# Optimization experiments

Measured on AMD Instinct MI355X. Metric: run time of the kernel, lower is better.

Reference implementation:

```python
import jax, jax.numpy as jnp
import numpy as np

N_NODES = 100000
N_EDGES = 1600000
DIM_IN = 128
DIM_OUT = 128


def setup_inputs() -> dict:
    key = jax.random.key(0)
    k_x, k_e, k_w = jax.random.split(key, 3)
    x = jax.random.normal(k_x, (N_NODES, DIM_IN), dtype=jnp.float32)
    edge_index = jax.random.randint(k_e, (2, N_EDGES), 0, N_NODES, dtype=jnp.int64)
    # Glorot-uniform weight like PyG's GCNConv linear layer, stored [d_in, d_out]
    limit = np.sqrt(6.0 / (DIM_IN + DIM_OUT)).astype(np.float32)
    W = jax.random.uniform(k_w, (DIM_IN, DIM_OUT), dtype=jnp.float32, minval=-limit, maxval=limit)
    return {"x": x, "edge_index": edge_index, "W": W}


def reference(x, edge_index, W):
    # PyG GCNConv (bias=False): out = D^{-1/2} (A + I) D^{-1/2} (x @ W)
    N = x.shape[0]
    x_proj = x @ W  # [N, d_out]
    loop = jnp.arange(N, dtype=edge_index.dtype)
    src = jnp.concatenate([edge_index[0], loop])  # message sources (row)
    dst = jnp.concatenate([edge_index[1], loop])  # aggregation targets (col)
    # degree counted at target nodes (edge weight = 1), incl. self loops
    deg = jax.ops.segment_sum(jnp.ones(src.shape, dtype=x.dtype), dst, num_segments=N)
    dis = jnp.where(deg > 0, jax.lax.rsqrt(deg), 0.0)
    norm = dis[src] * dis[dst]  # [E+N]
    msgs = x_proj[src] * norm[:, None]  # [E+N, d_out] gather + scale
    return jax.ops.segment_sum(msgs, dst, num_segments=N)  # scatter-add
```

## Files before the change

kernel.cpp:

```cpp
#include <hip/hip_runtime.h>
#include <hip/hip_bf16.h>

#define DIM 128
#define PCH 4096

typedef __attribute__((ext_vector_type(8))) short bf16x8;
typedef __attribute__((ext_vector_type(4))) float f32x4;

__device__ __forceinline__ float bfu_lo(unsigned u) { return __uint_as_float(u << 16); }
__device__ __forceinline__ float bfu_hi(unsigned u) { return __uint_as_float(u & 0xffff0000u); }
__device__ __forceinline__ unsigned short f2bf(float f) {
    unsigned u = __float_as_uint(f);
    u += 0x7fffu + ((u >> 16) & 1u);
    return (unsigned short)(u >> 16);
}

__device__ __forceinline__ int edge_at(const void* ei, int idx64, long long pos) {
    return idx64 ? (int)__builtin_nontemporal_load((const long long*)ei + pos)
                 : __builtin_nontemporal_load((const int*)ei + pos);
}

__global__ void init_detect(const unsigned* ei_w, int* flags, unsigned* bcnt, int E) {
    __shared__ unsigned s_or[256];
    int t = threadIdx.x;
    bcnt[t] = 0u;
    bcnt[256 + t] = 0u;
    unsigned o = 0;
    int lim = (E < 4096) ? E : 4096;
    for (int k = t; k < lim; k += 256) o |= ei_w[2 * k + 1];
    s_or[t] = o;
    __syncthreads();
    for (int s = 128; s > 0; s >>= 1) {
        if (t < s) s_or[t] |= s_or[t + s];
        __syncthreads();
    }
    if (t == 0) flags[0] = (s_or[0] == 0u) ? 1 : 0;
}

__global__ __launch_bounds__(256) void hist_pass(const void* ei, const int* flags,
                                                 unsigned* bcnt, int E, int shift) {
    __shared__ unsigned s_h[512];
    int t = threadIdx.x;
    for (int i = t; i < 512; i += 256) s_h[i] = 0u;
    __syncthreads();
    int idx64 = flags[0];
    long long stride = (long long)gridDim.x * 256;
    for (long long e = (long long)blockIdx.x * 256 + t; e < E; e += stride) {
        int d = edge_at(ei, idx64, (long long)E + e);
        atomicAdd(&s_h[d >> shift], 1u);
    }
    __syncthreads();
    for (int i = t; i < 512; i += 256)
        if (s_h[i]) atomicAdd(&bcnt[i], s_h[i]);
}

__global__ void scan_buckets(const unsigned* bcnt, unsigned* bbase, unsigned* bcur) {
    __shared__ unsigned wsum[8];
    int t = threadIdx.x;
    unsigned v = bcnt[t];
    unsigned s = v;
    int lane = t & 63;
#pragma unroll
    for (int off = 1; off < 64; off <<= 1) {
        unsigned u = __shfl_up(s, off, 64);
        if (lane >= off) s += u;
    }
    int w = t >> 6;
    if (lane == 63) wsum[w] = s;
    __syncthreads();
    unsigned woff = 0;
    for (int j = 0; j < w; j++) woff += wsum[j];
    unsigned excl = woff + s - v;
    bbase[t] = excl;
    bcur[t] = excl;
    if (t == 511) bbase[512] = excl + v;
}

__global__ __launch_bounds__(256) void partition(const void* ei, const int* flags,
                                                 unsigned* bcur, long long* pout,
                                                 int E, int B, int shift) {
    __shared__ unsigned s_hist[512], s_off[512], s_gbase[512], s_pref[512];
    __shared__ unsigned wsum[4];
    __shared__ long long s_p[PCH];
    int t = threadIdx.x;
    long long base = (long long)blockIdx.x * PCH;
    for (int i = t; i < 512; i += 256) { s_hist[i] = 0u; s_off[i] = 0u; }
    __syncthreads();
    int idx64 = flags[0];
    int d_[PCH / 256], s_[PCH / 256];
#pragma unroll 4
    for (int j = 0; j < PCH / 256; j++) {
        long long e = base + j * 256 + t;
        if (e < E) {
            d_[j] = edge_at(ei, idx64, (long long)E + e);
            s_[j] = edge_at(ei, idx64, e);
            atomicAdd(&s_hist[d_[j] >> shift], 1u);
        } else d_[j] = -1;
    }
    __syncthreads();
    unsigned v0 = s_hist[2 * t], v1 = s_hist[2 * t + 1];
    unsigned ps = v0 + v1;
    unsigned s = ps;
    int lane = t & 63;
#pragma unroll
    for (int off = 1; off < 64; off <<= 1) {
        unsigned u = __shfl_up(s, off, 64);
        if (lane >= off) s += u;
    }
    int w = t >> 6;
    if (lane == 63) wsum[w] = s;
    __syncthreads();
    unsigned woff = 0;
    for (int j = 0; j < w; j++) woff += wsum[j];
    unsigned excl = woff + s - ps;
    s_pref[2 * t] = excl;
    s_pref[2 * t + 1] = excl + v0;
    __syncthreads();
    for (int i = t; i < B; i += 256)
        if (s_hist[i]) s_gbase[i] = atomicAdd(&bcur[i], s_hist[i]);
#pragma unroll 4
    for (int j = 0; j < PCH / 256; j++)
        if (d_[j] >= 0) {
            int b = d_[j] >> shift;
            unsigned p = s_pref[b] + atomicAdd(&s_off[b], 1u);
            s_p[p] = ((long long)s_[j] << 32) | (unsigned)d_[j];
        }
    __syncthreads();
    long long rem = (long long)E - base;
    unsigned tot = (rem < PCH) ? (unsigned)rem : (unsigned)PCH;
    for (unsigned i = t; i < tot; i += 256) {
        int lo = 0, hi = B - 1;
        while (lo < hi) {
            int mid = (lo + hi + 1) >> 1;
            if (s_pref[mid] <= i) lo = mid; else hi = mid - 1;
        }
        pout[s_gbase[lo] + (i - s_pref[lo])] = s_p[i];
    }
}

__global__ __launch_bounds__(256) void build_csr(const long long* __restrict__ pairs,
                                                 const unsigned* __restrict__ bbase,
                                                 unsigned* deg, unsigned* row_start,
                                                 float* dis, int* col_src,
                                                 int N, int shift) {
    __shared__ unsigned cnt[512], cur[512], pref[512];
    __shared__ unsigned wsum[4];
    int b = blockIdx.x, t = threadIdx.x;
    int npb = 1 << shift;
    if (npb > 512) npb = 512;
    int nodeLo = b << shift;
    unsigned lo = bbase[b], hi = bbase[b + 1];
    for (int i = t; i < npb; i += 256) cnt[i] = 0u;
    __syncthreads();
    for (unsigned e = lo + t; e < hi; e += 256) {
        int d = (int)pairs[e];
        atomicAdd(&cnt[d - nodeLo], 1u);
    }
    __syncthreads();
    unsigned v0 = (2 * t < npb) ? cnt[2 * t] : 0u;
    unsigned v1 = (2 * t + 1 < npb) ? cnt[2 * t + 1] : 0u;
    unsigned ps = v0 + v1;
    unsigned s = ps;
    int lane = t & 63;
#pragma unroll
    for (int off = 1; off < 64; off <<= 1) {
        unsigned u = __shfl_up(s, off, 64);
        if (lane >= off) s += u;
    }
    int w = t >> 6;
    if (lane == 63) wsum[w] = s;
    __syncthreads();
    unsigned woff = 0;
    for (int j = 0; j < w; j++) woff += wsum[j];
    unsigned excl = woff + s - ps;
    if (2 * t < npb) pref[2 * t] = excl;
    if (2 * t + 1 < npb) pref[2 * t + 1] = excl + v0;
    __syncthreads();
    for (int i = t; i < npb; i += 256) {
        int node = nodeLo + i;
        unsigned rs = lo + pref[i];
        if (node < N) {
            unsigned c = cnt[i];
            deg[node] = c;
            row_start[node] = rs;
            dis[node] = rsqrtf((float)c + 1.0f);
        }
        cur[i] = rs;
    }
    __syncthreads();
    for (unsigned e = lo + t; e < hi; e += 256) {
        long long v = pairs[e];
        int d = (int)v;
        int sv = (int)(v >> 32);
        unsigned pos = atomicAdd(&cur[d - nodeLo], 1u);
        col_src[pos] = sv;
    }
}

__global__ void transposeW(const float* W, unsigned short* Wt) {
    int idx = blockIdx.x * 256 + threadIdx.x;
    if (idx < DIM * DIM) {
        int n = idx >> 7, k = idx & 127;
        Wt[idx] = f2bf(W[k * DIM + n]);
    }
}

__global__ __launch_bounds__(256) void gemm_xw(const float* __restrict__ x,
                                               const unsigned short* __restrict__ wt,
                                               const float* __restrict__ dis,
                                               unsigned short* __restrict__ xps, int N) {
    int tid = threadIdx.x;
    int wv = tid >> 6, lane = tid & 63;
    int l15 = lane & 15, quad = lane >> 4;
    int rowBase = blockIdx.x * 128 + wv * 32;

    f32x4 acc[2][8];
#pragma unroll
    for (int mt = 0; mt < 2; mt++)
#pragma unroll
        for (int nt = 0; nt < 8; nt++)
            acc[mt][nt] = (f32x4){0.f, 0.f, 0.f, 0.f};

#pragma unroll
    for (int k0 = 0; k0 < DIM; k0 += 32) {
        bf16x8 aa[2], bb[8];
#pragma unroll
        for (int mt = 0; mt < 2; mt++) {
            int r = rowBase + mt * 16 + l15;
            if (r > N - 1) r = N - 1;
            const float* xf = x + (size_t)r * DIM + k0 + quad * 8;
            float4 u0 = ((const float4*)xf)[0];
            float4 u1 = ((const float4*)xf)[1];
            bf16x8 a;
            a[0] = (short)f2bf(u0.x); a[1] = (short)f2bf(u0.y);
            a[2] = (short)f2bf(u0.z); a[3] = (short)f2bf(u0.w);
            a[4] = (short)f2bf(u1.x); a[5] = (short)f2bf(u1.y);
            a[6] = (short)f2bf(u1.z); a[7] = (short)f2bf(u1.w);
            aa[mt] = a;
        }
#pragma unroll
        for (int nt = 0; nt < 8; nt++)
            bb[nt] = *(const bf16x8*)(wt + (size_t)(nt * 16 + l15) * DIM + k0 + quad * 8);
#pragma unroll
        for (int mt = 0; mt < 2; mt++)
#pragma unroll
            for (int nt = 0; nt < 8; nt++)
                acc[mt][nt] = __builtin_amdgcn_mfma_f32_16x16x32_bf16(bb[nt], aa[mt], acc[mt][nt], 0, 0, 0);
    }

#pragma unroll
    for (int mt = 0; mt < 2; mt++) {
        int r = rowBase + mt * 16 + l15;
        if (r < N) {
            float sc = dis[r];
#pragma unroll
            for (int nt = 0; nt < 8; nt++) {
                int c0 = nt * 16 + quad * 4;
                ushort4 o;
                o.x = f2bf(acc[mt][nt][0] * sc);
                o.y = f2bf(acc[mt][nt][1] * sc);
                o.z = f2bf(acc[mt][nt][2] * sc);
                o.w = f2bf(acc[mt][nt][3] * sc);
                *(ushort4*)(xps + (size_t)r * DIM + c0) = o;
            }
        }
    }
}

__global__ __launch_bounds__(256) void aggregate(const unsigned short* __restrict__ xps,
                                                 const unsigned* __restrict__ row_start,
                                                 const unsigned* __restrict__ deg,
                                                 const float* __restrict__ dis,
                                                 const int* __restrict__ col_src,
                                                 float* __restrict__ out, int N) {
    int wid = (int)((blockIdx.x * 256 + threadIdx.x) >> 6);
    if (wid >= N) return;
    int lane = threadIdx.x & 63;
    int grp = lane >> 4, lin = lane & 15;
    const uint4* xp4 = (const uint4*)xps;

    float acc[8];
#pragma unroll
    for (int j = 0; j < 8; j++) acc[j] = 0.f;

    unsigned rs = row_start[wid];
    unsigned cnt = deg[wid];
    unsigned tot = cnt + 1;

    for (unsigned base = 0; base < tot; base += 64) {
        unsigned slot = base + (unsigned)lane;
        int idx = (slot < cnt) ? col_src[rs + slot] : wid;
        unsigned rem = tot - base; if (rem > 64) rem = 64;
        for (unsigned q = 0; q * 8 < rem; q++) {
            unsigned sl0 = q * 8 + (unsigned)grp;
            unsigned sl1 = sl0 + 4;
            int s0 = __shfl(idx, (int)sl0, 64);
            int s1 = __shfl(idx, (int)sl1, 64);
            float m0 = (sl0 < rem) ? 1.f : 0.f;
            float m1 = (sl1 < rem) ? 1.f : 0.f;
            uint4 v0 = xp4[(size_t)s0 * 16 + lin];
            uint4 v1 = xp4[(size_t)s1 * 16 + lin];
            acc[0] = fmaf(bfu_lo(v0.x), m0, acc[0]);
            acc[1] = fmaf(bfu_hi(v0.x), m0, acc[1]);
            acc[2] = fmaf(bfu_lo(v0.y), m0, acc[2]);
            acc[3] = fmaf(bfu_hi(v0.y), m0, acc[3]);
            acc[4] = fmaf(bfu_lo(v0.z), m0, acc[4]);
            acc[5] = fmaf(bfu_hi(v0.z), m0, acc[5]);
            acc[6] = fmaf(bfu_lo(v0.w), m0, acc[6]);
            acc[7] = fmaf(bfu_hi(v0.w), m0, acc[7]);
            acc[0] = fmaf(bfu_lo(v1.x), m1, acc[0]);
            acc[1] = fmaf(bfu_hi(v1.x), m1, acc[1]);
            acc[2] = fmaf(bfu_lo(v1.y), m1, acc[2]);
            acc[3] = fmaf(bfu_hi(v1.y), m1, acc[3]);
            acc[4] = fmaf(bfu_lo(v1.z), m1, acc[4]);
            acc[5] = fmaf(bfu_hi(v1.z), m1, acc[5]);
            acc[6] = fmaf(bfu_lo(v1.w), m1, acc[6]);
            acc[7] = fmaf(bfu_hi(v1.w), m1, acc[7]);
        }
    }

#pragma unroll
    for (int j = 0; j < 8; j++) {
        acc[j] += __shfl_xor(acc[j], 16, 64);
        acc[j] += __shfl_xor(acc[j], 32, 64);
    }

    float di = dis[wid];
    if (grp < 2) {
        int jb = (grp & 1) * 4;
        float4 o;
        o.x = acc[jb + 0] * di;
        o.y = acc[jb + 1] * di;
        o.z = acc[jb + 2] * di;
        o.w = acc[jb + 3] * di;
        *(float4*)(out + (size_t)wid * DIM + lin * 8 + jb) = o;
    }
}

extern "C" void kernel_launch(void* const* d_in, const int* in_sizes, int n_in,
                              void* d_out, int out_size, void* d_ws, size_t ws_size,
                              hipStream_t stream) {
    const int N = in_sizes[0] / DIM;
    const int E = in_sizes[1] / 2;
    const float* x = (const float*)d_in[0];
    const void* ei = d_in[1];
    const float* W = (const float*)d_in[2];
    float* out = (float*)d_out;

    int shift = 8;
    while ((((long long)N + (1LL << shift) - 1) >> shift) > 512 && shift < 9) shift++;
    int B = (int)(((long long)N + (1LL << shift) - 1) >> shift);

    char* wsp = (char*)d_ws;
    size_t off = 0;
    auto alloc = [&](size_t b) { void* p = wsp + off; off += (b + 255) & ~(size_t)255; return p; };
    int*      flags      = (int*)alloc(256);
    unsigned* bcnt       = (unsigned*)alloc(512 * 4);
    unsigned* bbase      = (unsigned*)alloc(513 * 4);
    unsigned* bcur       = (unsigned*)alloc(512 * 4);
    unsigned* deg        = (unsigned*)alloc((size_t)N * 4);
    unsigned* row_start  = (unsigned*)alloc((size_t)N * 4);
    float*    dis        = (float*)alloc((size_t)N * 4);
    int*      col_src    = (int*)alloc((size_t)E * 4);
    unsigned short* Wt   = (unsigned short*)alloc((size_t)DIM * DIM * 2);
    unsigned short* xps  = (unsigned short*)alloc((size_t)N * DIM * 2);

    long long* pairs = (long long*)xps;
    if ((size_t)E * 8 > (size_t)N * DIM * 2 && off + (size_t)E * 8 <= ws_size)
        pairs = (long long*)alloc((size_t)E * 8);

    init_detect<<<1, 256, 0, stream>>>((const unsigned*)ei, flags, bcnt, E);
    hist_pass<<<512, 256, 0, stream>>>(ei, flags, bcnt, E, shift);
    scan_buckets<<<1, 512, 0, stream>>>(bcnt, bbase, bcur);
    partition<<<(E + PCH - 1) / PCH, 256, 0, stream>>>(ei, flags, bcur, pairs, E, B, shift);
    build_csr<<<B, 256, 0, stream>>>(pairs, bbase, deg, row_start, dis, col_src, N, shift);
    transposeW<<<(DIM * DIM + 255) / 256, 256, 0, stream>>>(W, Wt);
    gemm_xw<<<(N + 127) / 128, 256, 0, stream>>>(x, Wt, dis, xps, N);
    aggregate<<<(N + 3) / 4, 256, 0, stream>>>(xps, row_start, deg, dis, col_src, out, N);
}
```

Before: 260.1 us.

## Fold detect, bucket scan and W transpose into neighbouring kernels

Removes the init_detect, scan_buckets and transposeW launches. The index-width detection is recomputed in every block of hist and partition, the bucket prefix scan is redone per block in partition and build_csr, and each gemm block transposes W to bf16 in padded shared memory. Counters are zeroed with a memset instead. This cuts launch and serialization gaps between small kernels at the cost of redundant per-block work: a 4096-element read and reduce, a 512-entry scan, and a 16K-element W conversion in every gemm block.

```diff
diff --git a/kernel.cpp b/kernel.cpp
--- a/kernel.cpp
+++ b/kernel.cpp
@@ -20,11 +20,9 @@
                  : __builtin_nontemporal_load((const int*)ei + pos);
 }
 
-__global__ void init_detect(const unsigned* ei_w, int* flags, unsigned* bcnt, int E) {
-    __shared__ unsigned s_or[256];
+__device__ __forceinline__ int detect_idx64(const void* ei, int E, unsigned* s_or, int* s_flag) {
+    const unsigned* ei_w = (const unsigned*)ei;
     int t = threadIdx.x;
-    bcnt[t] = 0u;
-    bcnt[256 + t] = 0u;
     unsigned o = 0;
     int lim = (E < 4096) ? E : 4096;
     for (int k = t; k < lim; k += 256) o |= ei_w[2 * k + 1];
@@ -34,16 +32,19 @@
         if (t < s) s_or[t] |= s_or[t + s];
         __syncthreads();
     }
-    if (t == 0) flags[0] = (s_or[0] == 0u) ? 1 : 0;
-}
-
-__global__ __launch_bounds__(256) void hist_pass(const void* ei, const int* flags,
-                                                 unsigned* bcnt, int E, int shift) {
+    if (t == 0) *s_flag = (s_or[0] == 0u) ? 1 : 0;
+    __syncthreads();
+    return *s_flag;
+}
+
+__global__ __launch_bounds__(256) void hist_detect(const void* ei, unsigned* bcnt,
+                                                   int E, int shift) {
     __shared__ unsigned s_h[512];
+    __shared__ unsigned s_or[256];
+    __shared__ int s_flag;
     int t = threadIdx.x;
     for (int i = t; i < 512; i += 256) s_h[i] = 0u;
-    __syncthreads();
-    int idx64 = flags[0];
+    int idx64 = detect_idx64(ei, E, s_or, &s_flag);
     long long stride = (long long)gridDim.x * 256;
     for (long long e = (long long)blockIdx.x * 256 + t; e < E; e += stride) {
         int d = edge_at(ei, idx64, (long long)E + e);
@@ -54,39 +55,40 @@
         if (s_h[i]) atomicAdd(&bcnt[i], s_h[i]);
 }
 
-__global__ void scan_buckets(const unsigned* bcnt, unsigned* bbase, unsigned* bcur) {
-    __shared__ unsigned wsum[8];
-    int t = threadIdx.x;
-    unsigned v = bcnt[t];
-    unsigned s = v;
-    int lane = t & 63;
-#pragma unroll
-    for (int off = 1; off < 64; off <<= 1) {
-        unsigned u = __shfl_up(s, off, 64);
-        if (lane >= off) s += u;
-    }
-    int w = t >> 6;
-    if (lane == 63) wsum[w] = s;
-    __syncthreads();
-    unsigned woff = 0;
-    for (int j = 0; j < w; j++) woff += wsum[j];
-    unsigned excl = woff + s - v;
-    bbase[t] = excl;
-    bcur[t] = excl;
-    if (t == 511) bbase[512] = excl + v;
-}
-
-__global__ __launch_bounds__(256) void partition(const void* ei, const int* flags,
-                                                 unsigned* bcur, long long* pout,
+__global__ __launch_bounds__(256) void partition(const void* ei, const unsigned* __restrict__ bcnt,
+                                                 unsigned* bcur0, long long* pout,
                                                  int E, int B, int shift) {
-    __shared__ unsigned s_hist[512], s_off[512], s_gbase[512], s_pref[512];
+    __shared__ unsigned s_hist[512], s_off[512], s_gbase[512], s_pref[512], s_bbase[512];
     __shared__ unsigned wsum[4];
+    __shared__ unsigned s_or[256];
+    __shared__ int s_flag;
     __shared__ long long s_p[PCH];
     int t = threadIdx.x;
     long long base = (long long)blockIdx.x * PCH;
     for (int i = t; i < 512; i += 256) { s_hist[i] = 0u; s_off[i] = 0u; }
-    __syncthreads();
-    int idx64 = flags[0];
+    int idx64 = detect_idx64(ei, E, s_or, &s_flag);
+
+    {
+        unsigned v0 = bcnt[2 * t], v1 = bcnt[2 * t + 1];
+        unsigned ps = v0 + v1;
+        unsigned s = ps;
+        int lane = t & 63;
+#pragma unroll
+        for (int off = 1; off < 64; off <<= 1) {
+            unsigned u = __shfl_up(s, off, 64);
+            if (lane >= off) s += u;
+        }
+        int w = t >> 6;
+        if (lane == 63) wsum[w] = s;
+        __syncthreads();
+        unsigned woff = 0;
+        for (int j = 0; j < w; j++) woff += wsum[j];
+        unsigned excl = woff + s - ps;
+        s_bbase[2 * t] = excl;
+        s_bbase[2 * t + 1] = excl + v0;
+    }
+    __syncthreads();
+
     int d_[PCH / 256], s_[PCH / 256];
 #pragma unroll 4
     for (int j = 0; j < PCH / 256; j++) {
@@ -98,26 +100,30 @@
         } else d_[j] = -1;
     }
     __syncthreads();
-    unsigned v0 = s_hist[2 * t], v1 = s_hist[2 * t + 1];
-    unsigned ps = v0 + v1;
-    unsigned s = ps;
-    int lane = t & 63;
-#pragma unroll
-    for (int off = 1; off < 64; off <<= 1) {
-        unsigned u = __shfl_up(s, off, 64);
-        if (lane >= off) s += u;
-    }
-    int w = t >> 6;
-    if (lane == 63) wsum[w] = s;
-    __syncthreads();
-    unsigned woff = 0;
-    for (int j = 0; j < w; j++) woff += wsum[j];
-    unsigned excl = woff + s - ps;
-    s_pref[2 * t] = excl;
-    s_pref[2 * t + 1] = excl + v0;
-    __syncthreads();
+
+    {
+        unsigned v0 = s_hist[2 * t], v1 = s_hist[2 * t + 1];
+        unsigned ps = v0 + v1;
+        unsigned s = ps;
+        int lane = t & 63;
+#pragma unroll
+        for (int off = 1; off < 64; off <<= 1) {
+            unsigned u = __shfl_up(s, off, 64);
+            if (lane >= off) s += u;
+        }
+        int w = t >> 6;
+        if (lane == 63) wsum[w] = s;
+        __syncthreads();
+        unsigned woff = 0;
+        for (int j = 0; j < w; j++) woff += wsum[j];
+        unsigned excl = woff + s - ps;
+        s_pref[2 * t] = excl;
+        s_pref[2 * t + 1] = excl + v0;
+    }
+    __syncthreads();
+
     for (int i = t; i < B; i += 256)
-        if (s_hist[i]) s_gbase[i] = atomicAdd(&bcur[i], s_hist[i]);
+        if (s_hist[i]) s_gbase[i] = s_bbase[i] + atomicAdd(&bcur0[i], s_hist[i]);
 #pragma unroll 4
     for (int j = 0; j < PCH / 256; j++)
         if (d_[j] >= 0) {
@@ -139,17 +145,41 @@
 }
 
 __global__ __launch_bounds__(256) void build_csr(const long long* __restrict__ pairs,
-                                                 const unsigned* __restrict__ bbase,
+                                                 const unsigned* __restrict__ bcnt,
                                                  unsigned* deg, unsigned* row_start,
                                                  float* dis, int* col_src,
                                                  int N, int shift) {
     __shared__ unsigned cnt[512], cur[512], pref[512];
+    __shared__ unsigned s_bb[513];
     __shared__ unsigned wsum[4];
     int b = blockIdx.x, t = threadIdx.x;
     int npb = 1 << shift;
     if (npb > 512) npb = 512;
     int nodeLo = b << shift;
-    unsigned lo = bbase[b], hi = bbase[b + 1];
+
+    {
+        unsigned v0 = bcnt[2 * t], v1 = bcnt[2 * t + 1];
+        unsigned ps = v0 + v1;
+        unsigned s = ps;
+        int lane = t & 63;
+#pragma unroll
+        for (int off = 1; off < 64; off <<= 1) {
+            unsigned u = __shfl_up(s, off, 64);
+            if (lane >= off) s += u;
+        }
+        int w = t >> 6;
+        if (lane == 63) wsum[w] = s;
+        __syncthreads();
+        unsigned woff = 0;
+        for (int j = 0; j < w; j++) woff += wsum[j];
+        unsigned excl = woff + s - ps;
+        s_bb[2 * t] = excl;
+        s_bb[2 * t + 1] = excl + v0;
+        if (t == 255) s_bb[512] = excl + ps;
+    }
+    __syncthreads();
+    unsigned lo = s_bb[b], hi = s_bb[b + 1];
+
     for (int i = t; i < npb; i += 256) cnt[i] = 0u;
     __syncthreads();
     for (unsigned e = lo + t; e < hi; e += 256) {
@@ -197,19 +227,18 @@
     }
 }
 
-__global__ void transposeW(const float* W, unsigned short* Wt) {
-    int idx = blockIdx.x * 256 + threadIdx.x;
-    if (idx < DIM * DIM) {
-        int n = idx >> 7, k = idx & 127;
-        Wt[idx] = f2bf(W[k * DIM + n]);
-    }
-}
-
 __global__ __launch_bounds__(256) void gemm_xw(const float* __restrict__ x,
-                                               const unsigned short* __restrict__ wt,
+                                               const float* __restrict__ W,
                                                const float* __restrict__ dis,
                                                unsigned short* __restrict__ xps, int N) {
+    __shared__ unsigned short wt[128 * 136];
     int tid = threadIdx.x;
+    for (int idx = tid; idx < DIM * DIM; idx += 256) {
+        int k = idx >> 7, n = idx & 127;
+        wt[n * 136 + k] = f2bf(W[idx]);
+    }
+    __syncthreads();
+
     int wv = tid >> 6, lane = tid & 63;
     int l15 = lane & 15, quad = lane >> 4;
     int rowBase = blockIdx.x * 128 + wv * 32;
@@ -240,7 +269,7 @@
         }
 #pragma unroll
         for (int nt = 0; nt < 8; nt++)
-            bb[nt] = *(const bf16x8*)(wt + (size_t)(nt * 16 + l15) * DIM + k0 + quad * 8);
+            bb[nt] = *(const bf16x8*)(wt + (nt * 16 + l15) * 136 + k0 + quad * 8);
 #pragma unroll
         for (int mt = 0; mt < 2; mt++)
 #pragma unroll
@@ -354,27 +383,22 @@
     char* wsp = (char*)d_ws;
     size_t off = 0;
     auto alloc = [&](size_t b) { void* p = wsp + off; off += (b + 255) & ~(size_t)255; return p; };
-    int*      flags      = (int*)alloc(256);
-    unsigned* bcnt       = (unsigned*)alloc(512 * 4);
-    unsigned* bbase      = (unsigned*)alloc(513 * 4);
-    unsigned* bcur       = (unsigned*)alloc(512 * 4);
+    unsigned* bcnt       = (unsigned*)alloc(4096);
+    unsigned* bcur0      = bcnt + 512;
     unsigned* deg        = (unsigned*)alloc((size_t)N * 4);
     unsigned* row_start  = (unsigned*)alloc((size_t)N * 4);
     float*    dis        = (float*)alloc((size_t)N * 4);
     int*      col_src    = (int*)alloc((size_t)E * 4);
-    unsigned short* Wt   = (unsigned short*)alloc((size_t)DIM * DIM * 2);
     unsigned short* xps  = (unsigned short*)alloc((size_t)N * DIM * 2);
 
     long long* pairs = (long long*)xps;
     if ((size_t)E * 8 > (size_t)N * DIM * 2 && off + (size_t)E * 8 <= ws_size)
         pairs = (long long*)alloc((size_t)E * 8);
 
-    init_detect<<<1, 256, 0, stream>>>((const unsigned*)ei, flags, bcnt, E);
-    hist_pass<<<512, 256, 0, stream>>>(ei, flags, bcnt, E, shift);
-    scan_buckets<<<1, 512, 0, stream>>>(bcnt, bbase, bcur);
-    partition<<<(E + PCH - 1) / PCH, 256, 0, stream>>>(ei, flags, bcur, pairs, E, B, shift);
-    build_csr<<<B, 256, 0, stream>>>(pairs, bbase, deg, row_start, dis, col_src, N, shift);
-    transposeW<<<(DIM * DIM + 255) / 256, 256, 0, stream>>>(W, Wt);
-    gemm_xw<<<(N + 127) / 128, 256, 0, stream>>>(x, Wt, dis, xps, N);
+    hipMemsetAsync(bcnt, 0, 4096, stream);
+    hist_detect<<<512, 256, 0, stream>>>(ei, bcnt, E, shift);
+    partition<<<(E + PCH - 1) / PCH, 256, 0, stream>>>(ei, bcnt, bcur0, pairs, E, B, shift);
+    build_csr<<<B, 256, 0, stream>>>(pairs, bcnt, deg, row_start, dis, col_src, N, shift);
+    gemm_xw<<<(N + 127) / 128, 256, 0, stream>>>(x, W, dis, xps, N);
     aggregate<<<(N + 3) / 4, 256, 0, stream>>>(xps, row_start, deg, dis, col_src, out, N);
 }
```

New measurement: 253.7 us. 1.03x faster.
